# Kernel tuning notes

Measured on AMD Instinct MI355X. Metric: run time of the kernel, lower is better.

The kernel has to match this reference:

```python
import jax, jax.numpy as jnp
import numpy as np

HID = 192
EPS = 1e-5

def _bn(x, g, b):
    # BatchNorm1d, training mode: batch stats over all leading axes, biased var
    ax = tuple(range(x.ndim - 1))
    m = x.mean(axis=ax)
    v = x.var(axis=ax)
    return (x - m) * jax.lax.rsqrt(v + EPS) * g + b

def _glorot(k, shape):
    lim = np.sqrt(6.0 / (shape[0] + shape[1]))
    return jax.random.uniform(k, shape, jnp.float32, -lim, lim)

def setup_inputs() -> dict:
    key = jax.random.key(0)
    ks = jax.random.split(key, 8)
    B, N, F, C = 16, 1024, 128, 10
    x = jax.random.normal(ks[0], (B, N, F), jnp.float32)
    adj = (jax.random.uniform(ks[1], (B, N, N)) < 0.01).astype(jnp.float32)
    adj = jnp.maximum(adj, jnp.swapaxes(adj, 1, 2))
    return dict(
        x=x, adj=adj,
        bn_feat_g=jnp.ones((F,), jnp.float32), bn_feat_b=jnp.full((F,), 1e-4, jnp.float32),
        W_feat=_glorot(ks[2], (F, HID)),
        bns_conv_g=jnp.ones((3, HID), jnp.float32), bns_conv_b=jnp.full((3, HID), 1e-4, jnp.float32),
        convs_W=jnp.stack([_glorot(jax.random.fold_in(ks[3], i), (HID, HID)) for i in range(3)]),
        convs_b=jnp.zeros((3, HID), jnp.float32),
        bn_fc_g=jnp.ones((HID,), jnp.float32), bn_fc_b=jnp.full((HID,), 1e-4, jnp.float32),
        lin_W=_glorot(ks[4], (HID, HID)), lin_b=jnp.zeros((HID,), jnp.float32),
        bn_hid_g=jnp.ones((HID,), jnp.float32), bn_hid_b=jnp.full((HID,), 1e-4, jnp.float32),
        cls_W=_glorot(ks[5], (HID, 10)), cls_b=jnp.zeros((10,), jnp.float32),
    )

def reference(x, adj, bn_feat_g, bn_feat_b, W_feat, bns_conv_g, bns_conv_b,
              convs_W, convs_b, bn_fc_g, bn_fc_b, lin_W, lin_b,
              bn_hid_g, bn_hid_b, cls_W, cls_b):
    B, N, _ = x.shape
    # dense_to_sparse discards edge values -> binary edges; add remaining self loops (weight 1)
    A = (adj != 0).astype(x.dtype)
    A = jnp.maximum(A, jnp.eye(N, dtype=x.dtype))
    deg = A.sum(-1)                                   # [B,N]
    dis = jnp.where(deg > 0, deg ** -0.5, 0.0)
    A_hat = dis[:, :, None] * A * dis[:, None, :]      # D^-1/2 (A+I) D^-1/2
    h = _bn(x, bn_feat_g, bn_feat_b)
    # conv_feat has gfn=True: pure linear transform, no bias, no propagation
    h = jax.nn.relu(jnp.einsum('bnf,fh->bnh', h, W_feat))
    for i in range(convs_W.shape[0]):
        h = _bn(h, bns_conv_g[i], bns_conv_b[i])
        h = jax.nn.relu(jnp.einsum('bij,bjh->bih', A_hat, h @ convs_W[i]) + convs_b[i])
    g = h.mean(axis=1)                                 # global_mean_pool -> [B,HID]
    g = _bn(g, bn_fc_g, bn_fc_b)
    g = jax.nn.relu(g @ lin_W + lin_b)
    g = _bn(g, bn_hid_g, bn_hid_b)
    logits = g @ cls_W + cls_b
    return jax.nn.log_softmax(logits, axis=-1)
```

## Files before the change

kernel.cpp:

```cpp
#include <hip/hip_runtime.h>
#include <hip/hip_bf16.h>

#define BB 16
#define NN 1024
#define FF 128
#define HH 192
#define NROWS (BB*NN)
#define MAXC 128
#define EPSV 1e-5f

constexpr size_t OFF_H0  = 0;
constexpr size_t OFF_ZB  = OFF_H0 + (size_t)NROWS*HH/2;
constexpr size_t OFF_WPF = OFF_ZB + (size_t)NROWS*HH/2;
constexpr size_t OFF_WPC = OFF_WPF + (size_t)HH*FF/2;
constexpr size_t OFF_BF  = OFF_WPC + (size_t)HH*HH/2;
constexpr size_t OFF_BC  = OFF_BF + HH;
constexpr size_t OFF_DIS = OFF_BC + HH;
constexpr size_t OFF_G   = OFF_DIS + NROWS;
constexpr size_t OFF_ST  = OFF_G + BB*HH;
constexpr size_t ST_SIZE = 512 + 3*8*512;
constexpr size_t OFF_FLAG= OFF_ST + ST_SIZE;
constexpr size_t OFF_CNT = OFF_FLAG + 1;
constexpr size_t OFF_COLS= OFF_CNT + NROWS;

typedef __attribute__((ext_vector_type(8))) short short8;
typedef __attribute__((ext_vector_type(4))) float f32x4;
typedef __attribute__((ext_vector_type(4))) unsigned int u32x4;
typedef __attribute__((ext_vector_type(2))) unsigned int u32x2;

static __device__ __forceinline__ float bf(const __hip_bfloat16 v) {
    return __bfloat162float(v);
}
static __device__ __forceinline__ float ldin(const void* p, size_t i, int isf) {
    return isf ? ((const float*)p)[i]
               : __bfloat162float(((const __hip_bfloat16*)p)[i]);
}
static __host__ __device__ __forceinline__ float* stage_h(float* ws, int s ) {
    return ws + OFF_ST + 512 + (size_t)s*8*512;
}
static __device__ __forceinline__ float blo(unsigned int u) {
    union { unsigned int x; float f; } v; v.x = u << 16; return v.f;
}
static __device__ __forceinline__ float bhi(unsigned int u) {
    union { unsigned int x; float f; } v; v.x = u & 0xFFFF0000u; return v.f;
}
static __device__ __forceinline__ unsigned int packbf(float a, float b) {
    union { unsigned int u; __hip_bfloat16 h[2]; } p;
    p.h[0] = __float2bfloat16(a); p.h[1] = __float2bfloat16(b);
    return p.u;
}

__global__ void detect_and_zero(const unsigned int* __restrict__ adjw, float* ws) {
    __shared__ int evid;
    int tid = threadIdx.x;
    if (tid == 0) evid = 0;
    __syncthreads();
    int local = 0;
    for (int k = tid; k < 16384; k += 256) {
        unsigned int w = adjw[k];
        if ((w & 0xFFFFu) == 0x3F80u) local++;
    }
    if (local) atomicAdd(&evid, local);
    for (size_t k = tid; k < ST_SIZE; k += 256) ws[OFF_ST + k] = 0.f;
    for (int k = tid; k < BB*HH; k += 256) ws[OFF_G + k] = 0.f;
    __syncthreads();
    if (tid == 0) ((int*)ws)[OFF_FLAG] = (evid == 0) ? 1 : 0;
}

__global__ __launch_bounds__(256) void phase1(const void* __restrict__ adj,
                                              const void* __restrict__ x, float* ws) {
    const int isf = ((const int*)ws)[OFF_FLAG];
    int tid = threadIdx.x;
    if (blockIdx.x < NROWS) {
        int row = blockIdx.x;
        int i   = row & (NN - 1);
        __shared__ int cnt_s;
        __shared__ unsigned short colbuf[MAXC];
        if (tid == 0) cnt_s = 0;
        __syncthreads();
        int j0 = tid*4;
        unsigned int bits[4];
        if (isf) {
            u32x4 v = *(const u32x4*)((const unsigned int*)adj + (size_t)row*NN + j0);
            bits[0]=v[0]; bits[1]=v[1]; bits[2]=v[2]; bits[3]=v[3];
        } else {
            u32x2 v = *(const u32x2*)((const unsigned short*)adj + (size_t)row*NN + j0);
            bits[0]=(v[0]&0xFFFFu); bits[1]=(v[0]>>16); bits[2]=(v[1]&0xFFFFu); bits[3]=(v[1]>>16);
        }
        #pragma unroll
        for (int e = 0; e < 4; ++e) {
            int j = j0 + e;
            if ((bits[e] << 1) != 0u || j == i) {
                int p = atomicAdd(&cnt_s, 1);
                if (p < MAXC) colbuf[p] = (unsigned short)j;
            }
        }
        __syncthreads();
        int c = cnt_s; if (c > MAXC) c = MAXC;
        if (tid == 0) {
            ((int*)(ws + OFF_CNT))[row] = c;
            ws[OFF_DIS + row] = rsqrtf((float)cnt_s);
        }
        unsigned short* cols = (unsigned short*)(ws + OFF_COLS);
        for (int k = tid; k < c; k += 256) cols[(size_t)row*MAXC + k] = colbuf[k];
    } else {
        int b2 = blockIdx.x - NROWS;
        int f = tid & (FF-1), half = tid >> 7;
        int r0 = b2*64 + half*32;
        float s = 0.f, sq = 0.f;
        for (int r = 0; r < 32; ++r) {
            float v = ldin(x, (size_t)(r0 + r)*FF + f, isf);
            s += v; sq += v*v;
        }
        atomicAdd(&ws[OFF_ST + f], s);
        atomicAdd(&ws[OFF_ST + 256 + f], sq);
    }
}

__global__ void prep_feat(const void* __restrict__ W_feat,
                          const void* __restrict__ gg, const void* __restrict__ bb,
                          float* ws) {
    const int isf = ((const int*)ws)[OFF_FLAG];
    int n = blockIdx.x, k = threadIdx.x;
    const float* st = ws + OFF_ST;
    float m   = st[k] * (1.f/NROWS);
    float var = st[256+k] * (1.f/NROWS) - m*m;
    float a   = ldin(gg, k, isf) * rsqrtf(var + EPSV);
    float c   = ldin(bb, k, isf) - m*a;
    float wv  = ldin(W_feat, (size_t)k*HH + n, isf);
    ((__hip_bfloat16*)(ws + OFF_WPF))[(size_t)n*FF + k] = __float2bfloat16(a*wv);
    __shared__ float red[FF];
    red[k] = c*wv;
    __syncthreads();
    for (int s = FF/2; s > 0; s >>= 1) {
        if (k < s) red[k] += red[k + s];
        __syncthreads();
    }
    if (k == 0) ws[OFF_BF + n] = red[0];
}

__global__ void prep_conv(const void* __restrict__ convs_W,
                          const void* __restrict__ gg, const void* __restrict__ bb,
                          int layer, float* ws) {
    const int isf = ((const int*)ws)[OFF_FLAG];
    int n = blockIdx.x, k = threadIdx.x;
    const float* st = stage_h(ws, layer);
    float s = 0.f, sq = 0.f;
    #pragma unroll
    for (int bkt = 0; bkt < 8; ++bkt) {
        s  += st[bkt*512 + k];
        sq += st[bkt*512 + 256 + k];
    }
    float m   = s * (1.f/NROWS);
    float var = sq * (1.f/NROWS) - m*m;
    float a   = ldin(gg, (size_t)layer*HH + k, isf) * rsqrtf(var + EPSV);
    float c   = ldin(bb, (size_t)layer*HH + k, isf) - m*a;
    float wv  = ldin(convs_W, (size_t)layer*HH*HH + (size_t)k*HH + n, isf);
    ((__hip_bfloat16*)(ws + OFF_WPC))[(size_t)n*HH + k] = __float2bfloat16(a*wv);
    __shared__ float red[HH];
    red[k] = c*wv;
    __syncthreads();
    if (k < 96) red[k] += red[k + 96];
    __syncthreads();
    for (int s2 = 48; s2 >= 3; s2 >>= 1) {
        if (k < s2) red[k] += red[k + s2];
        __syncthreads();
    }
    if (k == 0) ws[OFF_BC + n] = red[0] + red[1] + red[2];
}

template<int K, int MODE>
__global__ __launch_bounds__(256) void gemm_mfma(const void* __restrict__ A,
                                                 const __hip_bfloat16* __restrict__ BT,
                                                 const float* __restrict__ bias,
                                                 float* __restrict__ ws) {
    const int isf = ((const int*)ws)[OFF_FLAG];
    int lane = threadIdx.x & 63, w = threadIdx.x >> 6;
    int wr = w & 1, wc = w >> 1;
    int bi = blockIdx.x;
    int batch = bi & 15, seg = bi >> 4;
    int row0 = batch*NN + seg*32 + wr*16;
    int col0 = wc*96;
    int m    = lane & 15, quad = lane >> 4;
    f32x4 acc[6];
    #pragma unroll
    for (int t = 0; t < 6; ++t) acc[t] = f32x4{0.f,0.f,0.f,0.f};
    float bv[6];
    #pragma unroll
    for (int t = 0; t < 6; ++t) bv[t] = bias[col0 + t*16 + m];
    #pragma unroll
    for (int kb = 0; kb < K/32; ++kb) {
        short8 a;
        if (MODE == 0 && isf) {
            const float* Ar = (const float*)A + (size_t)(row0+m)*K + kb*32 + quad*8;
            f32x4 v0 = *(const f32x4*)Ar;
            f32x4 v1 = *(const f32x4*)(Ar + 4);
            union { short8 s8; __hip_bfloat16 h[8]; } u;
            #pragma unroll
            for (int e = 0; e < 4; ++e) {
                u.h[e]   = __float2bfloat16(v0[e]);
                u.h[e+4] = __float2bfloat16(v1[e]);
            }
            a = u.s8;
        } else {
            a = *(const short8*)((const __hip_bfloat16*)A +
                                 (size_t)(row0+m)*K + kb*32 + quad*8);
        }
        #pragma unroll
        for (int t = 0; t < 6; ++t) {
            short8 b = *(const short8*)(BT + (size_t)(col0 + t*16+m)*K + kb*32 + quad*8);
            acc[t] = __builtin_amdgcn_mfma_f32_16x16x32_bf16(a, b, acc[t], 0, 0, 0);
        }
    }
    if (MODE == 0) {
        __shared__ float sh[2*HH];
        for (int i = threadIdx.x; i < 2*HH; i += 256) sh[i] = 0.f;
        __syncthreads();
        __hip_bfloat16* H0 = (__hip_bfloat16*)(ws + OFF_H0);
        #pragma unroll
        for (int t = 0; t < 6; ++t) {
            int ch = col0 + t*16 + m;
            float s = 0.f, sq = 0.f;
            #pragma unroll
            for (int r = 0; r < 4; ++r) {
                float o = fmaxf(acc[t][r] + bv[t], 0.f);
                H0[(size_t)(row0 + quad*4 + r)*HH + ch] = __float2bfloat16(o);
                s += o; sq += o*o;
            }
            atomicAdd(&sh[ch], s);
            atomicAdd(&sh[HH + ch], sq);
        }
        __syncthreads();
        float* st = stage_h(ws, 0) + (bi & 7)*512;
        if (threadIdx.x < HH) {
            atomicAdd(&st[threadIdx.x], sh[threadIdx.x]);
            atomicAdd(&st[256 + threadIdx.x], sh[HH + threadIdx.x]);
        }
    } else {
        const float* dis = ws + OFF_DIS;
        __hip_bfloat16* Z = (__hip_bfloat16*)(ws + OFF_ZB);
        float sc[4];
        #pragma unroll
        for (int r = 0; r < 4; ++r) sc[r] = dis[row0 + quad*4 + r];
        #pragma unroll
        for (int t = 0; t < 6; ++t)
            #pragma unroll
            for (int r = 0; r < 4; ++r)
                Z[(size_t)(row0 + quad*4 + r)*HH + col0 + t*16 + m] =
                    __float2bfloat16((acc[t][r] + bv[t]) * sc[r]);
    }
}

__global__ __launch_bounds__(384) void spmm(const void* __restrict__ bias, int layer,
                                            float* __restrict__ stat_out, int is_pool,
                                            float* ws) {
    int tid = threadIdx.x;
    int rl  = tid / 96;
    int t   = tid - rl*96;
    const int isf = ((const int*)ws)[OFF_FLAG];
    int bi = blockIdx.x;
    int batch = bi & 15, seg = bi >> 4;
    int row  = batch*NN + seg*4 + rl;
    int base = batch*NN;
    const float* dis = ws + OFF_DIS;
    int c = ((const int*)(ws + OFF_CNT))[row];
    const unsigned short* cl = (const unsigned short*)(ws + OFF_COLS) + (size_t)row*MAXC;
    const unsigned int* Zu = (const unsigned int*)(ws + OFF_ZB);
    __shared__ float sh_s[HH];
    __shared__ float sh_q[HH];
    if (!is_pool) {
        for (int i = tid; i < HH; i += 384) { sh_s[i] = 0.f; sh_q[i] = 0.f; }
    } else {
        for (int i = tid; i < HH; i += 384) sh_s[i] = 0.f;
    }
    __syncthreads();
    float a0 = 0.f, a1 = 0.f;
    int k = 0;
    for (; k + 8 <= c; k += 8) {
        u32x4 cw = *(const u32x4*)(cl + k);
        int j[8];
        j[0] = (int)(cw[0] & 0xFFFFu); j[1] = (int)(cw[0] >> 16);
        j[2] = (int)(cw[1] & 0xFFFFu); j[3] = (int)(cw[1] >> 16);
        j[4] = (int)(cw[2] & 0xFFFFu); j[5] = (int)(cw[2] >> 16);
        j[6] = (int)(cw[3] & 0xFFFFu); j[7] = (int)(cw[3] >> 16);
        unsigned int z[8];
        #pragma unroll
        for (int e = 0; e < 8; ++e)
            z[e] = Zu[(size_t)(base + j[e])*96 + t];
        #pragma unroll
        for (int e = 0; e < 8; ++e) { a0 += blo(z[e]); a1 += bhi(z[e]); }
    }
    for (; k < c; ++k) {
        unsigned int z = Zu[(size_t)(base + (int)cl[k])*96 + t];
        a0 += blo(z); a1 += bhi(z);
    }
    float d  = dis[row];
    float b0 = ldin(bias, (size_t)layer*HH + 2*t,     isf);
    float b1 = ldin(bias, (size_t)layer*HH + 2*t + 1, isf);
    float o0 = fmaxf(d*a0 + b0, 0.f);
    float o1 = fmaxf(d*a1 + b1, 0.f);
    ((unsigned int*)(ws + OFF_H0))[(size_t)row*96 + t] = packbf(o0, o1);
    if (is_pool) {
        atomicAdd(&sh_s[2*t],     o0);
        atomicAdd(&sh_s[2*t + 1], o1);
        __syncthreads();
        if (tid < HH) atomicAdd(&ws[OFF_G + (size_t)batch*HH + tid], sh_s[tid]);
    } else {
        atomicAdd(&sh_s[2*t],     o0);
        atomicAdd(&sh_s[2*t + 1], o1);
        atomicAdd(&sh_q[2*t],     o0*o0);
        atomicAdd(&sh_q[2*t + 1], o1*o1);
        __syncthreads();
        float* st = stat_out + (bi & 7)*512;
        if (tid < HH) {
            atomicAdd(&st[tid],       sh_s[tid]);
            atomicAdd(&st[256 + tid], sh_q[tid]);
        }
    }
}

__global__ __launch_bounds__(768) void tail(
                     const void* __restrict__ fc_g,  const void* __restrict__ fc_b,
                     const void* __restrict__ lin_W, const void* __restrict__ lin_b,
                     const void* __restrict__ hid_g, const void* __restrict__ hid_b,
                     const void* __restrict__ cls_W, const void* __restrict__ cls_b,
                     void* __restrict__ out, const float* ws) {
    __shared__ float g1[BB][HH];
    __shared__ float g2[BB][HH];
    __shared__ __hip_bfloat16 Wl[HH*HH];
    __shared__ float logits[BB][10];
    __shared__ float lse[BB];
    int tid = threadIdx.x;
    const int isf = ((const int*)ws)[OFF_FLAG];
    const float* g = ws + OFF_G;
    if (isf) {
        const float* Wp = (const float*)lin_W;
        for (int i = tid; i < HH*HH; i += 768) Wl[i] = __float2bfloat16(Wp[i]);
    } else {
        const __hip_bfloat16* Wp = (const __hip_bfloat16*)lin_W;
        for (int i = tid; i < HH*HH; i += 768) Wl[i] = Wp[i];
    }
    if (tid < HH) {
        float s = 0.f, sq = 0.f;
        for (int b = 0; b < BB; ++b) {
            float v = g[b*HH + tid] * (1.f/NN);
            s += v; sq += v*v;
        }
        float m = s*(1.f/BB), var = sq*(1.f/BB) - m*m;
        float a = ldin(fc_g, tid, isf) * rsqrtf(var + EPSV);
        float c = ldin(fc_b, tid, isf) - m*a;
        for (int b = 0; b < BB; ++b) g1[b][tid] = g[b*HH + tid]*(1.f/NN)*a + c;
    }
    __syncthreads();
    {
        int n = tid % HH, bg = tid / HH;
        float lb = ldin(lin_b, n, isf);
        float a0 = lb, a1 = lb, a2 = lb, a3 = lb;
        int b0 = bg*4;
        for (int k = 0; k < HH; ++k) {
            float wv = bf(Wl[k*HH + n]);
            a0 += g1[b0+0][k]*wv;
            a1 += g1[b0+1][k]*wv;
            a2 += g1[b0+2][k]*wv;
            a3 += g1[b0+3][k]*wv;
        }
        g2[b0+0][n] = fmaxf(a0, 0.f);
        g2[b0+1][n] = fmaxf(a1, 0.f);
        g2[b0+2][n] = fmaxf(a2, 0.f);
        g2[b0+3][n] = fmaxf(a3, 0.f);
    }
    __syncthreads();
    if (tid < HH) {
        float s = 0.f, sq = 0.f;
        for (int b = 0; b < BB; ++b) { float v = g2[b][tid]; s += v; sq += v*v; }
        float m = s*(1.f/BB), var = sq*(1.f/BB) - m*m;
        float a = ldin(hid_g, tid, isf) * rsqrtf(var + EPSV);
        float c = ldin(hid_b, tid, isf) - m*a;
        for (int b = 0; b < BB; ++b) g2[b][tid] = g2[b][tid]*a + c;
    }
    __syncthreads();
    if (tid < BB*10) {
        int b = tid/10, k = tid%10;
        float acc = ldin(cls_b, k, isf);
        for (int h = 0; h < HH; ++h) acc += g2[b][h] * ldin(cls_W, (size_t)h*10 + k, isf);
        logits[b][k] = acc;
    }
    __syncthreads();
    if (tid < BB) {
        float m = -1e30f;
        for (int k = 0; k < 10; ++k) m = fmaxf(m, logits[tid][k]);
        float s = 0.f;
        for (int k = 0; k < 10; ++k) s += expf(logits[tid][k] - m);
        lse[tid] = m + logf(s);
    }
    __syncthreads();
    if (tid < BB*10) {
        int b = tid/10;
        float v = logits[b][tid%10] - lse[b];
        if (isf) ((float*)out)[tid] = v;
        else     ((__hip_bfloat16*)out)[tid] = __float2bfloat16(v);
    }
}

extern "C" void kernel_launch(void* const* d_in, const int* in_sizes, int n_in,
                              void* d_out, int out_size, void* d_ws, size_t ws_size,
                              hipStream_t stream) {
    const void* x       = d_in[0];
    const void* adj     = d_in[1];
    const void* bnf_g   = d_in[2];
    const void* bnf_b   = d_in[3];
    const void* W_feat  = d_in[4];
    const void* bnc_g   = d_in[5];
    const void* bnc_b   = d_in[6];
    const void* convs_W = d_in[7];
    const void* convs_b = d_in[8];
    const void* fc_g    = d_in[9];
    const void* fc_b    = d_in[10];
    const void* lin_W   = d_in[11];
    const void* lin_b   = d_in[12];
    const void* hid_g   = d_in[13];
    const void* hid_b   = d_in[14];
    const void* cls_W   = d_in[15];
    const void* cls_b   = d_in[16];

    float* ws = (float*)d_ws;
    const __hip_bfloat16* WPF = (const __hip_bfloat16*)(ws + OFF_WPF);
    const __hip_bfloat16* WPC = (const __hip_bfloat16*)(ws + OFF_WPC);

    detect_and_zero<<<1, 256, 0, stream>>>((const unsigned int*)adj, ws);
    phase1<<<NROWS + 256, 256, 0, stream>>>(adj, x, ws);
    prep_feat<<<HH, FF, 0, stream>>>(W_feat, bnf_g, bnf_b, ws);
    gemm_mfma<FF, 0><<<NROWS/32, 256, 0, stream>>>(x, WPF, ws + OFF_BF, ws);
    for (int l = 0; l < 3; ++l) {
        prep_conv<<<HH, HH, 0, stream>>>(convs_W, bnc_g, bnc_b, l, ws);
        gemm_mfma<HH, 1><<<NROWS/32, 256, 0, stream>>>(
            (const void*)(ws + OFF_H0), WPC, ws + OFF_BC, ws);
        spmm<<<NROWS/4, 384, 0, stream>>>(convs_b, l,
            (l < 2) ? stage_h(ws, l + 1) : nullptr, (l == 2) ? 1 : 0, ws);
    }
    tail<<<1, 768, 0, stream>>>(fc_g, fc_b, lin_W, lin_b,
                                hid_g, hid_b, cls_W, cls_b, d_out, ws);
}
```

Before: 356.3 us.

## Stage per-batch Z column slice in LDS and gather neighbours from shared memory

The SpMM kernel is restructured so each block owns one batch graph and a 32-column slice of the hidden dimension. The block first copies that slice of Z for all 1024 nodes into 64KB of LDS, then aggregates 512 rows per block by gathering neighbours from LDS instead of doing scattered global loads. Statistics are reduced in registers and with wave shuffles, replacing shared-memory atomics. The grid drops from 4096 blocks to 192 with large LDS use, which lowers occupancy and parallelism, and the Z slice is re-read once per half-block.

```diff
diff --git a/kernel.cpp b/kernel.cpp
--- a/kernel.cpp
+++ b/kernel.cpp
@@ -251,70 +251,93 @@
     }
 }
 
-__global__ __launch_bounds__(384) void spmm(const void* __restrict__ bias, int layer,
+__global__ __launch_bounds__(512) void spmm(const void* __restrict__ bias, int layer,
                                             float* __restrict__ stat_out, int is_pool,
                                             float* ws) {
+    __shared__ unsigned int Zs[NN*16];
+    const int isf = ((const int*)ws)[OFF_FLAG];
     int tid = threadIdx.x;
-    int rl  = tid / 96;
-    int t   = tid - rl*96;
-    const int isf = ((const int*)ws)[OFF_FLAG];
     int bi = blockIdx.x;
-    int batch = bi & 15, seg = bi >> 4;
-    int row  = batch*NN + seg*4 + rl;
-    int base = batch*NN;
+    int batch = bi & 15;
+    int rest  = bi >> 4;
+    int slice = rest % 6;
+    int half  = rest / 6;
+    int c0 = slice*32;
+    const unsigned int* Zu = (const unsigned int*)(ws + OFF_ZB)
+                             + (size_t)batch*NN*96 + c0/2;
+    for (int i = tid; i < NN*16; i += 512) {
+        int r = i >> 4, u = i & 15;
+        Zs[i] = Zu[(size_t)r*96 + u];
+    }
+    __syncthreads();
+    int d = tid & 7, rslot = tid >> 3;
     const float* dis = ws + OFF_DIS;
-    int c = ((const int*)(ws + OFF_CNT))[row];
-    const unsigned short* cl = (const unsigned short*)(ws + OFF_COLS) + (size_t)row*MAXC;
-    const unsigned int* Zu = (const unsigned int*)(ws + OFF_ZB);
-    __shared__ float sh_s[HH];
-    __shared__ float sh_q[HH];
-    if (!is_pool) {
-        for (int i = tid; i < HH; i += 384) { sh_s[i] = 0.f; sh_q[i] = 0.f; }
-    } else {
-        for (int i = tid; i < HH; i += 384) sh_s[i] = 0.f;
-    }
-    __syncthreads();
-    float a0 = 0.f, a1 = 0.f;
-    int k = 0;
-    for (; k + 8 <= c; k += 8) {
-        u32x4 cw = *(const u32x4*)(cl + k);
-        int j[8];
-        j[0] = (int)(cw[0] & 0xFFFFu); j[1] = (int)(cw[0] >> 16);
-        j[2] = (int)(cw[1] & 0xFFFFu); j[3] = (int)(cw[1] >> 16);
-        j[4] = (int)(cw[2] & 0xFFFFu); j[5] = (int)(cw[2] >> 16);
-        j[6] = (int)(cw[3] & 0xFFFFu); j[7] = (int)(cw[3] >> 16);
-        unsigned int z[8];
-        #pragma unroll
-        for (int e = 0; e < 8; ++e)
-            z[e] = Zu[(size_t)(base + j[e])*96 + t];
-        #pragma unroll
-        for (int e = 0; e < 8; ++e) { a0 += blo(z[e]); a1 += bhi(z[e]); }
-    }
-    for (; k < c; ++k) {
-        unsigned int z = Zu[(size_t)(base + (int)cl[k])*96 + t];
-        a0 += blo(z); a1 += bhi(z);
-    }
-    float d  = dis[row];
-    float b0 = ldin(bias, (size_t)layer*HH + 2*t,     isf);
-    float b1 = ldin(bias, (size_t)layer*HH + 2*t + 1, isf);
-    float o0 = fmaxf(d*a0 + b0, 0.f);
-    float o1 = fmaxf(d*a1 + b1, 0.f);
-    ((unsigned int*)(ws + OFF_H0))[(size_t)row*96 + t] = packbf(o0, o1);
-    if (is_pool) {
-        atomicAdd(&sh_s[2*t],     o0);
-        atomicAdd(&sh_s[2*t + 1], o1);
-        __syncthreads();
-        if (tid < HH) atomicAdd(&ws[OFF_G + (size_t)batch*HH + tid], sh_s[tid]);
-    } else {
-        atomicAdd(&sh_s[2*t],     o0);
-        atomicAdd(&sh_s[2*t + 1], o1);
-        atomicAdd(&sh_q[2*t],     o0*o0);
-        atomicAdd(&sh_q[2*t + 1], o1*o1);
-        __syncthreads();
-        float* st = stat_out + (bi & 7)*512;
-        if (tid < HH) {
-            atomicAdd(&st[tid],       sh_s[tid]);
-            atomicAdd(&st[256 + tid], sh_q[tid]);
+    const int* cnt = (const int*)(ws + OFF_CNT);
+    const unsigned short* cols = (const unsigned short*)(ws + OFF_COLS);
+    unsigned int* H0u = (unsigned int*)(ws + OFF_H0);
+    float bch[4];
+    #pragma unroll
+    for (int e = 0; e < 4; ++e)
+        bch[e] = ldin(bias, (size_t)layer*HH + c0 + d*4 + e, isf);
+    float s_acc[4] = {0.f,0.f,0.f,0.f}, q_acc[4] = {0.f,0.f,0.f,0.f};
+    for (int it = 0; it < 8; ++it) {
+        int row = batch*NN + half*512 + it*64 + rslot;
+        int c = cnt[row];
+        const unsigned short* cl = cols + (size_t)row*MAXC;
+        float a0=0.f, a1=0.f, a2=0.f, a3=0.f;
+        int k = 0;
+        for (; k + 8 <= c; k += 8) {
+            u32x4 cw = *(const u32x4*)(cl + k);
+            int j[8];
+            j[0]=(int)(cw[0]&0xFFFFu); j[1]=(int)(cw[0]>>16);
+            j[2]=(int)(cw[1]&0xFFFFu); j[3]=(int)(cw[1]>>16);
+            j[4]=(int)(cw[2]&0xFFFFu); j[5]=(int)(cw[2]>>16);
+            j[6]=(int)(cw[3]&0xFFFFu); j[7]=(int)(cw[3]>>16);
+            u32x2 z[8];
+            #pragma unroll
+            for (int e = 0; e < 8; ++e)
+                z[e] = *(const u32x2*)(&Zs[j[e]*16 + d*2]);
+            #pragma unroll
+            for (int e = 0; e < 8; ++e) {
+                a0 += blo(z[e][0]); a1 += bhi(z[e][0]);
+                a2 += blo(z[e][1]); a3 += bhi(z[e][1]);
+            }
+        }
+        for (; k < c; ++k) {
+            u32x2 z = *(const u32x2*)(&Zs[(int)cl[k]*16 + d*2]);
+            a0 += blo(z[0]); a1 += bhi(z[0]);
+            a2 += blo(z[1]); a3 += bhi(z[1]);
+        }
+        float dd = dis[row];
+        float o0 = fmaxf(dd*a0 + bch[0], 0.f);
+        float o1 = fmaxf(dd*a1 + bch[1], 0.f);
+        float o2 = fmaxf(dd*a2 + bch[2], 0.f);
+        float o3 = fmaxf(dd*a3 + bch[3], 0.f);
+        u32x2 outw; outw[0] = packbf(o0,o1); outw[1] = packbf(o2,o3);
+        *(u32x2*)(&H0u[(size_t)row*96 + c0/2 + d*2]) = outw;
+        s_acc[0]+=o0; s_acc[1]+=o1; s_acc[2]+=o2; s_acc[3]+=o3;
+        q_acc[0]+=o0*o0; q_acc[1]+=o1*o1; q_acc[2]+=o2*o2; q_acc[3]+=o3*o3;
+    }
+    #pragma unroll
+    for (int e = 0; e < 4; ++e) {
+        #pragma unroll
+        for (int mask = 8; mask < 64; mask <<= 1) {
+            s_acc[e] += __shfl_xor(s_acc[e], mask, 64);
+            q_acc[e] += __shfl_xor(q_acc[e], mask, 64);
+        }
+    }
+    if ((tid & 63) < 8) {
+        if (is_pool) {
+            #pragma unroll
+            for (int e = 0; e < 4; ++e)
+                atomicAdd(&ws[OFF_G + (size_t)batch*HH + c0 + d*4 + e], s_acc[e]);
+        } else {
+            float* st = stat_out + (bi & 7)*512;
+            #pragma unroll
+            for (int e = 0; e < 4; ++e) {
+                atomicAdd(&st[c0 + d*4 + e],       s_acc[e]);
+                atomicAdd(&st[256 + c0 + d*4 + e], q_acc[e]);
+            }
         }
     }
 }
@@ -435,7 +458,7 @@
         prep_conv<<<HH, HH, 0, stream>>>(convs_W, bnc_g, bnc_b, l, ws);
         gemm_mfma<HH, 1><<<NROWS/32, 256, 0, stream>>>(
             (const void*)(ws + OFF_H0), WPC, ws + OFF_BC, ws);
-        spmm<<<NROWS/4, 384, 0, stream>>>(convs_b, l,
+        spmm<<<192, 512, 0, stream>>>(convs_b, l,
             (l < 2) ? stage_h(ws, l + 1) : nullptr, (l == 2) ? 1 : 0, ws);
     }
     tail<<<1, 768, 0, stream>>>(fc_g, fc_b, lin_W, lin_b,
```

Result: faster. 331.7 us (-6.9%).
